# Optimization experiments

Measured on AMD Instinct MI355X. Metric: run time of the kernel, lower is better.

## Reference

```python
import jax, jax.numpy as jnp
import numpy as np

# QuantumConv2d from ESPCN-PyTorch (quantum variant).
# QuantumLinear(kH, kW, ...) is a parameterized quantum circuit mapping a flattened
# kH*kW patch to kH Z-expectation values. We model the standard single-qubit-per-row
# RY-chain circuit: out[k] = cos( sum_w patch[k, w] + theta[k] )  (Z expectation after
# sequential RY rotations by the kW row inputs plus one trainable angle per row).
# The conv then averages the kH outputs and sums over input channels, exactly as the
# torch forward does. We replicate the original's circuits[i*j] indexing (i=out ch,
# j=in ch), and use cos(a+b)=cos a cos b - sin a sin b to turn the channel/row
# reduction into two dense einsums (same math, efficient expression).

KH, KW = 3, 3
PH, PW = 1, 1
OC = 32


def setup_inputs() -> dict:
    key = jax.random.key(0)
    k1, k2 = jax.random.split(key)
    x = jax.random.normal(k1, (8, 16, 128, 128), dtype=jnp.float32)
    # one circuit per (out_ch, in_ch, kernel_row): oC*iC*kH = 32*16*3 = 1536, kH params each
    theta = jax.random.normal(k2, (OC * 16 * KH, KH), dtype=jnp.float32)
    return {"x": x, "theta": theta}


def _row_window_sums(x):
    # x: (n, iC, H, W) -> (n, iC, kH, oH, oW): sum over the kW window for each kernel row
    xp = jnp.pad(x, ((0, 0), (0, 0), (PH, PH), (PW, PW)))
    Hp, Wp = xp.shape[2], xp.shape[3]
    oH, oW = Hp - (KH - 1), Wp - (KW - 1)
    rows = []
    for k in range(KH):  # tiny fixed loop over kernel rows
        s = xp[:, :, k:k + oH, 0:oW]
        for w in range(1, KW):
            s = s + xp[:, :, k:k + oH, w:w + oW]
        rows.append(s)
    return jnp.stack(rows, axis=2)


def reference(x, theta):
    n, iC = x.shape[0], x.shape[1]
    R = _row_window_sums(x)  # (n, iC, kH, oH, oW) angle sums per patch row
    # replicate torch's self.circuits[i * j] lookup
    idx = jnp.arange(OC)[:, None] * jnp.arange(iC)[None, :]  # (oC, iC)
    th = theta[idx]  # (oC, iC, kH)
    # out[n,i,h,w] = sum_j mean_k cos(R[n,j,k,h,w] + th[i,j,k])
    out = (jnp.einsum('njkhw,ijk->nihw', jnp.cos(R), jnp.cos(th))
           - jnp.einsum('njkhw,ijk->nihw', jnp.sin(R), jnp.sin(th))) / KH
    return out
```

## Files before the change

kernel.cpp:

```cpp
#include <hip/hip_runtime.h>

#define OC 32
#define IC 16
#define HH 128
#define WW 128
#define NB 8
#define NG 4
#define CPG (OC / NG)
#define NM (IC * 3)

__global__ __launch_bounds__(256, 4) void qconv_kernel(
        const float* __restrict__ x,
        const float* __restrict__ theta,
        float* __restrict__ out) {
    __shared__ float cw_s[NM * OC];
    __shared__ float sw_s[NM * OC];

    int t = threadIdx.y * 64 + threadIdx.x;
#pragma unroll
    for (int q = t; q < NM * OC; q += 256) {
        int m = q >> 5;
        int i = q & 31;
        int j = m / 3;
        int k = m - j * 3;
        float v = theta[(i * j) * 3 + k];
        float sn, cs;
        __sincosf(v, &sn, &cs);
        cw_s[q] = cs;
        sw_s[q] = -sn;
    }
    __syncthreads();

    int bid = blockIdx.x;
    int wbase = (bid & 1) * 64;
    int hp = (bid >> 1) & 63;
    int n = bid >> 7;
    int h0 = hp * 2;
    int w = wbase + threadIdx.x;
    int g = threadIdx.y;

    float acc0[CPG], acc1[CPG];
#pragma unroll
    for (int c = 0; c < CPG; ++c) { acc0[c] = 0.f; acc1[c] = 0.f; }

    const float* xn = x + (size_t)n * IC * HH * WW;
    const float* cwg = cw_s + g * CPG;
    const float* swg = sw_s + g * CPG;

    bool wl = (w > 0), wr = (w < WW - 1);

#pragma unroll 2
    for (int j = 0; j < IC; ++j) {
        const float* xj = xn + j * HH * WW;
        float rs[4];
#pragma unroll
        for (int tt = 0; tt < 4; ++tt) {
            int r = h0 - 1 + tt;
            float s = 0.f;
            if (r >= 0 && r < HH) {
                const float* row = xj + r * WW;
                float c0 = row[w];
                float cm = wl ? row[w - 1] : 0.f;
                float cp = wr ? row[w + 1] : 0.f;
                s = cm + c0 + cp;
            }
            rs[tt] = s;
        }
        float sn[4], cs[4];
#pragma unroll
        for (int tt = 0; tt < 4; ++tt) __sincosf(rs[tt], &sn[tt], &cs[tt]);

#pragma unroll
        for (int k = 0; k < 3; ++k) {
            int m = j * 3 + k;
            const float4* c4 = (const float4*)(cwg + m * OC);
            const float4* s4 = (const float4*)(swg + m * OC);
            float cs0 = cs[k], sn0 = sn[k];
            float cs1 = cs[k + 1], sn1 = sn[k + 1];
#pragma unroll
            for (int q = 0; q < 2; ++q) {
                float4 cc = c4[q];
                float4 ss = s4[q];
                acc0[4*q+0] = fmaf(cs0, cc.x, fmaf(sn0, ss.x, acc0[4*q+0]));
                acc0[4*q+1] = fmaf(cs0, cc.y, fmaf(sn0, ss.y, acc0[4*q+1]));
                acc0[4*q+2] = fmaf(cs0, cc.z, fmaf(sn0, ss.z, acc0[4*q+2]));
                acc0[4*q+3] = fmaf(cs0, cc.w, fmaf(sn0, ss.w, acc0[4*q+3]));
                acc1[4*q+0] = fmaf(cs1, cc.x, fmaf(sn1, ss.x, acc1[4*q+0]));
                acc1[4*q+1] = fmaf(cs1, cc.y, fmaf(sn1, ss.y, acc1[4*q+1]));
                acc1[4*q+2] = fmaf(cs1, cc.z, fmaf(sn1, ss.z, acc1[4*q+2]));
                acc1[4*q+3] = fmaf(cs1, cc.w, fmaf(sn1, ss.w, acc1[4*q+3]));
            }
        }
    }

    const float inv3 = 1.0f / 3.0f;
    float* outp = out + ((size_t)n * OC + g * CPG) * HH * WW + (size_t)h0 * WW + w;
#pragma unroll
    for (int c = 0; c < CPG; ++c) {
        outp[(size_t)c * HH * WW]      = acc0[c] * inv3;
        outp[(size_t)c * HH * WW + WW] = acc1[c] * inv3;
    }
}

extern "C" void kernel_launch(void* const* d_in, const int* in_sizes, int n_in,
                              void* d_out, int out_size, void* d_ws, size_t ws_size,
                              hipStream_t stream) {
    const float* x     = (const float*)d_in[0];
    const float* theta = (const float*)d_in[1];
    float* out = (float*)d_out;

    dim3 block(64, NG, 1);
    int nblocks = NB * (HH / 2) * 2;
    qconv_kernel<<<nblocks, block, 0, stream>>>(x, theta, out);
}
```

Baseline: 85.52 us.

## Share per-row sincos across channel-group warps via LDS staging

Before, each of the four warps (one per output-channel group) loaded the same four input rows and computed the same sincos values for every input channel, so that work ran four times over. Now each warp handles one of the four rows: it computes the 3-wide window sum and its sincos for 8 channels at a time and writes the result to shared memory. After a barrier, all warps read the shared values to accumulate their output channels. The cos/-sin weights are also interleaved into float2 pairs. In exchange the kernel uses more LDS per block and adds barriers per half of the channels.

```diff
diff --git a/kernel.cpp b/kernel.cpp
--- a/kernel.cpp
+++ b/kernel.cpp
@@ -8,15 +8,26 @@
 #define NG 4
 #define CPG (OC / NG)
 #define NM (IC * 3)
+#define JH 8
 
 __global__ __launch_bounds__(256, 4) void qconv_kernel(
         const float* __restrict__ x,
         const float* __restrict__ theta,
         float* __restrict__ out) {
-    __shared__ float cw_s[NM * OC];
-    __shared__ float sw_s[NM * OC];
+    __shared__ float2 wgt_s[NM * OC];
+    __shared__ float2 trig_s[4][JH][64];
 
-    int t = threadIdx.y * 64 + threadIdx.x;
+    int tx = threadIdx.x;
+    int ty = threadIdx.y;
+    int t = ty * 64 + tx;
+
+    int bid = blockIdx.x;
+    int wbase = (bid & 1) * 64;
+    int hp = (bid >> 1) & 63;
+    int n = bid >> 7;
+    int h0 = hp * 2;
+    int w = wbase + tx;
+
 #pragma unroll
     for (int q = t; q < NM * OC; q += 256) {
         int m = q >> 5;
@@ -26,75 +37,63 @@
         float v = theta[(i * j) * 3 + k];
         float sn, cs;
         __sincosf(v, &sn, &cs);
-        cw_s[q] = cs;
-        sw_s[q] = -sn;
+        wgt_s[q] = make_float2(cs, -sn);
     }
-    __syncthreads();
 
-    int bid = blockIdx.x;
-    int wbase = (bid & 1) * 64;
-    int hp = (bid >> 1) & 63;
-    int n = bid >> 7;
-    int h0 = hp * 2;
-    int w = wbase + threadIdx.x;
-    int g = threadIdx.y;
+    const float* xn = x + (size_t)n * IC * HH * WW;
+    int r = h0 - 1 + ty;
+    bool valid = (r >= 0) && (r < HH);
+    bool wl = (w > 0), wr = (w < WW - 1);
 
     float acc0[CPG], acc1[CPG];
 #pragma unroll
     for (int c = 0; c < CPG; ++c) { acc0[c] = 0.f; acc1[c] = 0.f; }
 
-    const float* xn = x + (size_t)n * IC * HH * WW;
-    const float* cwg = cw_s + g * CPG;
-    const float* swg = sw_s + g * CPG;
-
-    bool wl = (w > 0), wr = (w < WW - 1);
-
-#pragma unroll 2
-    for (int j = 0; j < IC; ++j) {
-        const float* xj = xn + j * HH * WW;
-        float rs[4];
-#pragma unroll
-        for (int tt = 0; tt < 4; ++tt) {
-            int r = h0 - 1 + tt;
+    for (int half = 0; half < 2; ++half) {
+        if (half) __syncthreads();
+#pragma unroll 4
+        for (int jj = 0; jj < JH; ++jj) {
+            int j = half * JH + jj;
             float s = 0.f;
-            if (r >= 0 && r < HH) {
-                const float* row = xj + r * WW;
+            if (valid) {
+                const float* row = xn + ((size_t)j * HH + r) * WW;
                 float c0 = row[w];
                 float cm = wl ? row[w - 1] : 0.f;
                 float cp = wr ? row[w + 1] : 0.f;
                 s = cm + c0 + cp;
             }
-            rs[tt] = s;
+            float sn, cs;
+            __sincosf(s, &sn, &cs);
+            trig_s[ty][jj][tx] = make_float2(cs, sn);
         }
-        float sn[4], cs[4];
+        __syncthreads();
+
+#pragma unroll 2
+        for (int jj = 0; jj < JH; ++jj) {
+            int j = half * JH + jj;
+            float2 v0 = trig_s[0][jj][tx];
+            float2 v1 = trig_s[1][jj][tx];
+            float2 v2 = trig_s[2][jj][tx];
+            float2 v3 = trig_s[3][jj][tx];
+            float csA[4] = {v0.x, v1.x, v2.x, v3.x};
+            float snA[4] = {v0.y, v1.y, v2.y, v3.y};
 #pragma unroll
-        for (int tt = 0; tt < 4; ++tt) __sincosf(rs[tt], &sn[tt], &cs[tt]);
-
+            for (int k = 0; k < 3; ++k) {
+                const float2* wm = wgt_s + (j * 3 + k) * OC + ty * CPG;
+                float cs0 = csA[k],     sn0 = snA[k];
+                float cs1 = csA[k + 1], sn1 = snA[k + 1];
 #pragma unroll
-        for (int k = 0; k < 3; ++k) {
-            int m = j * 3 + k;
-            const float4* c4 = (const float4*)(cwg + m * OC);
-            const float4* s4 = (const float4*)(swg + m * OC);
-            float cs0 = cs[k], sn0 = sn[k];
-            float cs1 = cs[k + 1], sn1 = sn[k + 1];
-#pragma unroll
-            for (int q = 0; q < 2; ++q) {
-                float4 cc = c4[q];
-                float4 ss = s4[q];
-                acc0[4*q+0] = fmaf(cs0, cc.x, fmaf(sn0, ss.x, acc0[4*q+0]));
-                acc0[4*q+1] = fmaf(cs0, cc.y, fmaf(sn0, ss.y, acc0[4*q+1]));
-                acc0[4*q+2] = fmaf(cs0, cc.z, fmaf(sn0, ss.z, acc0[4*q+2]));
-                acc0[4*q+3] = fmaf(cs0, cc.w, fmaf(sn0, ss.w, acc0[4*q+3]));
-                acc1[4*q+0] = fmaf(cs1, cc.x, fmaf(sn1, ss.x, acc1[4*q+0]));
-                acc1[4*q+1] = fmaf(cs1, cc.y, fmaf(sn1, ss.y, acc1[4*q+1]));
-                acc1[4*q+2] = fmaf(cs1, cc.z, fmaf(sn1, ss.z, acc1[4*q+2]));
-                acc1[4*q+3] = fmaf(cs1, cc.w, fmaf(sn1, ss.w, acc1[4*q+3]));
+                for (int c = 0; c < CPG; ++c) {
+                    float2 wv = wm[c];
+                    acc0[c] = fmaf(cs0, wv.x, fmaf(sn0, wv.y, acc0[c]));
+                    acc1[c] = fmaf(cs1, wv.x, fmaf(sn1, wv.y, acc1[c]));
+                }
             }
         }
     }
 
     const float inv3 = 1.0f / 3.0f;
-    float* outp = out + ((size_t)n * OC + g * CPG) * HH * WW + (size_t)h0 * WW + w;
+    float* outp = out + ((size_t)n * OC + ty * CPG) * HH * WW + (size_t)h0 * WW + w;
 #pragma unroll
     for (int c = 0; c < CPG; ++c) {
         outp[(size_t)c * HH * WW]      = acc0[c] * inv3;
```

Result: faster. 82.90 us (-3.1%).
